# Optimization experiments

Hardware: AMD Instinct MI355X
Metric: run time of the kernel (lower is better)

The kernel has to match this reference:

```python
import jax, jax.numpy as jnp
import numpy as np

B, C_IN, C_OUT, STYLE_DIM, H, W = 8, 512, 512, 512, 32, 32

def setup_inputs() -> dict:
    key = jax.random.key(0)
    k = jax.random.split(key, 7)
    x = jax.random.normal(k[0], (B, C_IN, H, W), dtype=jnp.float32)
    style = jax.random.normal(k[1], (B, STYLE_DIM), dtype=jnp.float32)
    noise = jax.random.normal(k[2], (B, 1, 2 * H, 2 * W), dtype=jnp.float32)
    # learned params (Conv2d weight, style_fc Linear, output bias)
    conv_w = jax.random.normal(k[3], (C_OUT, C_IN, 3, 3), dtype=jnp.float32) * 0.05
    fc_w = jax.random.normal(k[4], (C_IN, STYLE_DIM), dtype=jnp.float32) * 0.05
    fc_b = jax.random.normal(k[5], (C_IN,), dtype=jnp.float32) * 0.05
    bias = jnp.zeros((1, C_OUT, 1, 1), dtype=jnp.float32)
    return {"x": x, "style": style, "noise": noise,
            "conv_w": conv_w, "fc_w": fc_w, "fc_b": fc_b, "bias": bias}

def reference(x, style, noise, conv_w, fc_w, fc_b, bias):
    b, c, h, w = x.shape
    o = conv_w.shape[0]
    x = jnp.repeat(jnp.repeat(x, 2, axis=2), 2, axis=3)  # (B, C, 2H, 2W)
    # style modulation: (B, C)
    s = style @ fc_w.T + fc_b
    # per-sample modulated weight (B, O, C, 3, 3)
    wmod = conv_w[None] * (s[:, None, :, None, None] + 1.0)
    # demodulation
    d = jax.lax.rsqrt(jnp.sum(wmod * wmod, axis=(2, 3, 4)) + 1e-8)  # (B, O)
    wmod = wmod * d[:, :, None, None, None]
    # grouped conv: one group per batch sample
    xr = x.reshape(1, b * c, 2 * h, 2 * w)
    wr = wmod.reshape(b * o, c, 3, 3)
    y = jax.lax.conv_general_dilated(
        xr, wr, window_strides=(1, 1), padding='SAME',
        feature_group_count=b,
        dimension_numbers=('NCHW', 'OIHW', 'NCHW'))
    y = y.reshape(b, o, 2 * h, 2 * w) + bias + noise
    return jax.nn.leaky_relu(y, negative_slope=0.2)
```

## Files before the change

### kernel.cpp

```cpp
#include <hip/hip_runtime.h>

typedef short v8s __attribute__((ext_vector_type(8)));
typedef float f32x4 __attribute__((ext_vector_type(4)));
typedef unsigned short ushort_t;

#define BB    8
#define CIN   512
#define COUT  512
#define SDIM  512

#define GLDS(g, l)                                                      \
    __builtin_amdgcn_global_load_lds(                                   \
        (const __attribute__((address_space(1))) void*)(g),             \
        (__attribute__((address_space(3))) void*)(l), 16, 0, 0)

static __device__ __forceinline__ ushort_t f2bf(float f) {
    union { float f; unsigned u; } un; un.f = f;
    unsigned r = un.u + 0x7FFF + ((un.u >> 16) & 1);
    return (ushort_t)(r >> 16);
}

__global__ void k_prep1(const float* __restrict__ style, const float* __restrict__ fc_w,
                        const float* __restrict__ fc_b, float* __restrict__ m,
                        const float* __restrict__ conv_w, float* __restrict__ q,
                        ushort_t* __restrict__ Wb, float* __restrict__ guard) {
    __shared__ float sst[SDIM];
    const int bid = blockIdx.x;
    if (bid < 1024) {
        const int idx = bid * 256 + threadIdx.x;
        const int o = idx >> 9, c = idx & 511;
        float w[3][3];
        const float* wp = conv_w + idx * 9;
        float qs = 0.f;
        for (int i = 0; i < 3; i++)
            for (int j = 0; j < 3; j++) {
                float v = wp[i * 3 + j];
                w[i][j] = v;
                qs += v * v;
            }
        q[idx] = qs;
        const int ch = c >> 5, kg = (c >> 3) & 3, c8 = c & 7;
        for (int py = 0; py < 2; py++) {
            float rs[2][3];
            for (int kx = 0; kx < 3; kx++) {
                rs[0][kx] = (py == 0) ? w[0][kx] : w[0][kx] + w[1][kx];
                rs[1][kx] = (py == 0) ? w[1][kx] + w[2][kx] : w[2][kx];
            }
            for (int px = 0; px < 2; px++) {
                const int p = py * 2 + px;
                float vals[4];
                if (px == 0) {
                    vals[0] = rs[0][0];
                    vals[1] = rs[0][1] + rs[0][2];
                    vals[2] = rs[1][0];
                    vals[3] = rs[1][1] + rs[1][2];
                } else {
                    vals[0] = rs[0][0] + rs[0][1];
                    vals[1] = rs[0][2];
                    vals[2] = rs[1][0] + rs[1][1];
                    vals[3] = rs[1][2];
                }
                for (int t = 0; t < 4; t++)
                    Wb[(size_t)p * (16 * 4 * 4 * 512 * 8) + (size_t)ch * (4 * 4 * 512 * 8)
                       + ((size_t)(t * 4 + kg) * 512 + o) * 8 + c8] = f2bf(vals[t]);
            }
        }
    } else {
        const int sb = bid - 1024;
        const int bx = sb & 1, b = sb >> 1;
        if (sb == 0 && threadIdx.x < 8) guard[threadIdx.x] = 0.f;
        for (int k = threadIdx.x; k < SDIM; k += 256) sst[k] = style[b * SDIM + k];
        __syncthreads();
        const int c = bx * 256 + threadIdx.x;
        float acc = fc_b[c];
        const float* wr = fc_w + c * SDIM;
        for (int k = 0; k < SDIM; k += 4) {
            float4 w4 = *(const float4*)(wr + k);
            acc += w4.x * sst[k] + w4.y * sst[k + 1] + w4.z * sst[k + 2] + w4.w * sst[k + 3];
        }
        m[b * CIN + c] = acc + 1.0f;
    }
}

__global__ void k_prep2(const float* __restrict__ x, const float* __restrict__ m,
                        ushort_t* __restrict__ Xt, const float* __restrict__ q,
                        float* __restrict__ d) {
    __shared__ __align__(16) ushort_t lt[32 * 528];
    const int bid = blockIdx.x, t = threadIdx.x;
    if (bid < 256) {
        const int r = bid & 31, b = bid >> 5;
        for (int s = t; s < 4096; s += 256) {
            const int c = s >> 3, q4 = (s & 7) * 4;
            float4 v = *(const float4*)(x + (((size_t)(b * CIN + c) * 32 + r) * 32 + q4));
            const float mv = m[b * CIN + c];
            lt[(q4 + 0) * 528 + c] = f2bf(v.x * mv);
            lt[(q4 + 1) * 528 + c] = f2bf(v.y * mv);
            lt[(q4 + 2) * 528 + c] = f2bf(v.z * mv);
            lt[(q4 + 3) * 528 + c] = f2bf(v.w * mv);
        }
        __syncthreads();
        for (int s = t; s < 2048; s += 256) {
            const int qq = s >> 6, c8 = s & 63;
            v8s v = *(v8s*)&lt[qq * 528 + c8 * 8];
            *(v8s*)(Xt + (((size_t)(b * 32 + r) * 32 + qq) * 512 + c8 * 8)) = v;
        }
    } else {
        const int w = (bid - 256) * 4 + (t >> 6);
        const int L = t & 63;
        const int b = w >> 9, o = w & 511;
        float4 q1 = *(const float4*)(q + o * 512 + L * 8);
        float4 q2 = *(const float4*)(q + o * 512 + L * 8 + 4);
        float4 m1 = *(const float4*)(m + b * 512 + L * 8);
        float4 m2 = *(const float4*)(m + b * 512 + L * 8 + 4);
        float acc = m1.x * m1.x * q1.x + m1.y * m1.y * q1.y + m1.z * m1.z * q1.z +
                    m1.w * m1.w * q1.w + m2.x * m2.x * q2.x + m2.y * m2.y * q2.y +
                    m2.z * m2.z * q2.z + m2.w * m2.w * q2.w;
        for (int off = 32; off; off >>= 1) acc += __shfl_down(acc, off, 64);
        if (L == 0) d[w] = rsqrtf(acc + 1e-8f);
    }
}

__global__ __launch_bounds__(256, 2) void k_gemm(
    const ushort_t* __restrict__ Xt, const ushort_t* __restrict__ Wb,
    const float* __restrict__ dmod, const float* __restrict__ bias,
    const float* __restrict__ noise, float* __restrict__ out,
    const float* __restrict__ guard) {
    __shared__ __align__(16) ushort_t Wt[2][128 * 64];
    __shared__ __align__(16) ushort_t Xs[2][128 * 64];

    const int tid = threadIdx.x;
    const int L = tid & 63;
    const int wid = tid >> 6;

    const int lin = blockIdx.x + 4 * blockIdx.y + 32 * blockIdx.z;
    const int log = (lin & 7) * 128 + (lin >> 3);
    const int o0 = (log & 3) * 128;
    const int r0 = ((log >> 2) & 7) * 4;
    const int zz = log >> 5;
    const int b = zz >> 2, p = zz & 3;

    const int py = p >> 1, px = p & 1;
    const int ry0 = py ? 0 : -1, cx0 = px ? 0 : -1;
    const int wo = (wid >> 1) * 64, wn = (wid & 1) * 64;
    const int l15 = L & 15, l4 = L >> 4;

    const ushort_t* XtB = Xt + (size_t)b * (32 * 32 * 512);
    const ushort_t* WbP = Wb + (size_t)p * (16 * 4 * 4 * 512 * 8);

    f32x4 acc[4][4];
#pragma unroll
    for (int i = 0; i < 4; i++)
#pragma unroll
        for (int j = 0; j < 4; j++) acc[i][j] = {0.f, 0.f, 0.f, 0.f};

    auto stage = [&](int c0, ushort_t* wbuf, ushort_t* xbuf) {
#pragma unroll
        for (int i = 0; i < 4; i++) {
            const int slot0 = i * 256 + (tid & 192);
            const int slot = i * 256 + tid;
            const int row = slot >> 3;
            const int k16 = (slot & 7) ^ (row & 7);
            const int tp = k16 >> 1;
            const int cg = c0 + (k16 & 1) * 8;
            const ushort_t* wsrc =
                WbP + (size_t)(cg >> 5) * (4 * 4 * 512 * 8)
                + ((size_t)((tp * 4 + ((cg >> 3) & 3)) * 512 + o0 + row)) * 8;
            GLDS(wsrc, wbuf + (size_t)slot0 * 8);
            const int gr = r0 + (row >> 5) + ry0 + (tp >> 1);
            const int gq = (row & 31) + cx0 + (tp & 1);
            const ushort_t* xsrc =
                ((unsigned)gr < 32u && (unsigned)gq < 32u)
                    ? XtB + (size_t)((gr * 32 + gq) * 512 + cg)
                    : (const ushort_t*)guard;
            GLDS(xsrc, xbuf + (size_t)slot0 * 8);
        }
    };

    stage(0, Wt[0], Xs[0]);
    __syncthreads();

    const int swz = (l15 & 7) << 3;
    int cur = 0;
    for (int c0 = 0; c0 < CIN; c0 += 16) {
        if (c0 + 16 < CIN) stage(c0 + 16, Wt[cur ^ 1], Xs[cur ^ 1]);
        const ushort_t* wbuf = Wt[cur];
        const ushort_t* xbuf = Xs[cur];
#pragma unroll
        for (int s = 0; s < 2; s++) {
            const int ko = (s * 32 + l4 * 8) ^ swz;
            v8s af[4], bfr[4];
#pragma unroll
            for (int i = 0; i < 4; i++)
                af[i] = *(const v8s*)&wbuf[(wo + i * 16 + l15) * 64 + ko];
#pragma unroll
            for (int j = 0; j < 4; j++)
                bfr[j] = *(const v8s*)&xbuf[(wn + j * 16 + l15) * 64 + ko];
#pragma unroll
            for (int i = 0; i < 4; i++)
#pragma unroll
                for (int j = 0; j < 4; j++)
                    acc[i][j] = __builtin_amdgcn_mfma_f32_16x16x32_bf16(
                        af[i], bfr[j], acc[i][j], 0, 0, 0);
        }
        __syncthreads();
        cur ^= 1;
    }

    const float* db = dmod + b * COUT;
    float nz[4];
    int ooff[4];
#pragma unroll
    for (int j = 0; j < 4; j++) {
        const int n = wn + j * 16 + l15;
        const int Y = 2 * (r0 + (n >> 5)) + py, X = 2 * (n & 31) + px;
        nz[j] = noise[b * 4096 + Y * 64 + X];
        ooff[j] = Y * 64 + X;
    }
    float* outB = out + (size_t)b * COUT * 4096;
#pragma unroll
    for (int i = 0; i < 4; i++) {
        const int ob = o0 + wo + i * 16 + l4 * 4;
        float4 d4 = *(const float4*)(db + ob);
        float4 b4 = *(const float4*)(bias + ob);
        const float dv[4] = {d4.x, d4.y, d4.z, d4.w};
        const float bv[4] = {b4.x, b4.y, b4.z, b4.w};
#pragma unroll
        for (int reg = 0; reg < 4; reg++) {
            float* orow = outB + (size_t)(ob + reg) * 4096;
#pragma unroll
            for (int j = 0; j < 4; j++) {
                float v = acc[i][j][reg] * dv[reg] + bv[reg] + nz[j];
                orow[ooff[j]] = v > 0.f ? v : 0.2f * v;
            }
        }
    }
}

extern "C" void kernel_launch(void* const* d_in, const int* in_sizes, int n_in,
                              void* d_out, int out_size, void* d_ws, size_t ws_size,
                              hipStream_t stream) {
    const float* x      = (const float*)d_in[0];
    const float* style  = (const float*)d_in[1];
    const float* noise  = (const float*)d_in[2];
    const float* conv_w = (const float*)d_in[3];
    const float* fc_w   = (const float*)d_in[4];
    const float* fc_b   = (const float*)d_in[5];
    const float* bias   = (const float*)d_in[6];
    float* out = (float*)d_out;

    float* ws = (float*)d_ws;
    float* m     = ws;
    float* dmod  = ws + 4096;
    float* q     = ws + 8192;
    float* guard = ws + 270336;
    ushort_t* XtU = (ushort_t*)(ws + 270352);
    ushort_t* WbU = XtU + 4194304;

    k_prep1<<<1040, 256, 0, stream>>>(style, fc_w, fc_b, m, conv_w, q, WbU, guard);
    k_prep2<<<1280, 256, 0, stream>>>(x, m, XtU, q, dmod);
    k_gemm<<<dim3(4, 8, 32), 256, 0, stream>>>(XtU, WbU, dmod, bias, noise, out, guard);
}
```

Measured before the change: 226.6 us.

## Enlarge GEMM tiles to 256x256 with 32x32 MFMA and interleaved staging

```diff
diff --git a/kernel.cpp b/kernel.cpp
--- a/kernel.cpp
+++ b/kernel.cpp
@@ -2,6 +2,7 @@
 
 typedef short v8s __attribute__((ext_vector_type(8)));
 typedef float f32x4 __attribute__((ext_vector_type(4)));
+typedef float f32x16 __attribute__((ext_vector_type(16)));
 typedef unsigned short ushort_t;
 
 #define BB    8
@@ -120,117 +121,146 @@
     }
 }
 
-__global__ __launch_bounds__(256, 2) void k_gemm(
+__global__ __launch_bounds__(512, 2) void k_gemm(
     const ushort_t* __restrict__ Xt, const ushort_t* __restrict__ Wb,
     const float* __restrict__ dmod, const float* __restrict__ bias,
     const float* __restrict__ noise, float* __restrict__ out,
     const float* __restrict__ guard) {
-    __shared__ __align__(16) ushort_t Wt[2][128 * 64];
-    __shared__ __align__(16) ushort_t Xs[2][128 * 64];
+    __shared__ __align__(16) ushort_t Wt[2][256 * 64];
+    __shared__ __align__(16) ushort_t Xs[2][256 * 64];
 
     const int tid = threadIdx.x;
     const int L = tid & 63;
     const int wid = tid >> 6;
 
-    const int lin = blockIdx.x + 4 * blockIdx.y + 32 * blockIdx.z;
-    const int log = (lin & 7) * 128 + (lin >> 3);
-    const int o0 = (log & 3) * 128;
-    const int r0 = ((log >> 2) & 7) * 4;
-    const int zz = log >> 5;
+    const int lin = blockIdx.x + 2 * blockIdx.y + 8 * blockIdx.z;
+    const int log = (lin & 7) * 32 + (lin >> 3);
+    const int o0 = (log & 1) * 256;
+    const int n0 = ((log >> 1) & 3) * 256;
+    const int zz = log >> 3;
     const int b = zz >> 2, p = zz & 3;
 
     const int py = p >> 1, px = p & 1;
     const int ry0 = py ? 0 : -1, cx0 = px ? 0 : -1;
-    const int wo = (wid >> 1) * 64, wn = (wid & 1) * 64;
-    const int l15 = L & 15, l4 = L >> 4;
+    const int wo = (wid >> 2) * 128, wn = (wid & 3) * 64;
+    const int l31 = L & 31, h = L >> 5;
 
     const ushort_t* XtB = Xt + (size_t)b * (32 * 32 * 512);
     const ushort_t* WbP = Wb + (size_t)p * (16 * 4 * 4 * 512 * 8);
 
-    f32x4 acc[4][4];
+    f32x16 acc[4][2];
 #pragma unroll
     for (int i = 0; i < 4; i++)
 #pragma unroll
-        for (int j = 0; j < 4; j++) acc[i][j] = {0.f, 0.f, 0.f, 0.f};
-
-    auto stage = [&](int c0, ushort_t* wbuf, ushort_t* xbuf) {
+        for (int j = 0; j < 2; j++)
+#pragma unroll
+            for (int r = 0; r < 16; r++) acc[i][j][r] = 0.f;
+
+    auto stage_w = [&](int c0, ushort_t* wbuf) {
 #pragma unroll
         for (int i = 0; i < 4; i++) {
-            const int slot0 = i * 256 + (tid & 192);
-            const int slot = i * 256 + tid;
+            const int slot = i * 512 + tid;
             const int row = slot >> 3;
-            const int k16 = (slot & 7) ^ (row & 7);
-            const int tp = k16 >> 1;
-            const int cg = c0 + (k16 & 1) * 8;
+            const int g = (slot & 7) ^ (row & 7);
+            const int tap = g >> 1;
+            const int cg = c0 + (g & 1) * 8;
             const ushort_t* wsrc =
                 WbP + (size_t)(cg >> 5) * (4 * 4 * 512 * 8)
-                + ((size_t)((tp * 4 + ((cg >> 3) & 3)) * 512 + o0 + row)) * 8;
-            GLDS(wsrc, wbuf + (size_t)slot0 * 8);
-            const int gr = r0 + (row >> 5) + ry0 + (tp >> 1);
-            const int gq = (row & 31) + cx0 + (tp & 1);
+                + ((size_t)((tap * 4 + ((cg >> 3) & 3)) * 512 + o0 + row)) * 8;
+            GLDS(wsrc, wbuf + (size_t)(i * 512 + (tid & 448)) * 8);
+        }
+    };
+    auto stage_x = [&](int c0, ushort_t* xbuf) {
+#pragma unroll
+        for (int i = 0; i < 4; i++) {
+            const int slot = i * 512 + tid;
+            const int row = slot >> 3;
+            const int g = (slot & 7) ^ (row & 7);
+            const int tap = g >> 1;
+            const int cg = c0 + (g & 1) * 8;
+            const int pix = n0 + row;
+            const int gr = (pix >> 5) + ry0 + (tap >> 1);
+            const int gq = (pix & 31) + cx0 + (tap & 1);
             const ushort_t* xsrc =
                 ((unsigned)gr < 32u && (unsigned)gq < 32u)
                     ? XtB + (size_t)((gr * 32 + gq) * 512 + cg)
                     : (const ushort_t*)guard;
-            GLDS(xsrc, xbuf + (size_t)slot0 * 8);
+            GLDS(xsrc, xbuf + (size_t)(i * 512 + (tid & 448)) * 8);
         }
     };
 
-    stage(0, Wt[0], Xs[0]);
+    stage_w(0, Wt[0]);
+    stage_x(0, Xs[0]);
+    asm volatile("s_waitcnt vmcnt(0)" ::: "memory");
     __syncthreads();
 
-    const int swz = (l15 & 7) << 3;
     int cur = 0;
-    for (int c0 = 0; c0 < CIN; c0 += 16) {
-        if (c0 + 16 < CIN) stage(c0 + 16, Wt[cur ^ 1], Xs[cur ^ 1]);
-        const ushort_t* wbuf = Wt[cur];
-        const ushort_t* xbuf = Xs[cur];
-#pragma unroll
-        for (int s = 0; s < 2; s++) {
-            const int ko = (s * 32 + l4 * 8) ^ swz;
-            v8s af[4], bfr[4];
+    for (int t = 0; t < 32; ++t) {
+        const ushort_t* wb = Wt[cur];
+        const ushort_t* xb = Xs[cur];
+        const int c0n = (t + 1) * 16;
+#pragma unroll
+        for (int s = 0; s < 4; ++s) {
+            v8s af[4], bfr[2];
+            const int ga = (2 * s + h) ^ (l31 & 7);
+#pragma unroll
+            for (int i = 0; i < 4; i++) {
+                const int row = wo + i * 32 + l31;
+                af[i] = *(const v8s*)&wb[row * 64 + ga * 8];
+            }
+#pragma unroll
+            for (int j = 0; j < 2; j++) {
+                const int row = wn + j * 32 + l31;
+                bfr[j] = *(const v8s*)&xb[row * 64 + ga * 8];
+            }
+            if (t < 31) {
+                if (s == 0) stage_w(c0n, Wt[cur ^ 1]);
+                else if (s == 1) stage_x(c0n, Xs[cur ^ 1]);
+            }
+            __builtin_amdgcn_s_barrier();
+            __builtin_amdgcn_s_setprio(1);
 #pragma unroll
             for (int i = 0; i < 4; i++)
-                af[i] = *(const v8s*)&wbuf[(wo + i * 16 + l15) * 64 + ko];
-#pragma unroll
-            for (int j = 0; j < 4; j++)
-                bfr[j] = *(const v8s*)&xbuf[(wn + j * 16 + l15) * 64 + ko];
-#pragma unroll
-            for (int i = 0; i < 4; i++)
-#pragma unroll
-                for (int j = 0; j < 4; j++)
-                    acc[i][j] = __builtin_amdgcn_mfma_f32_16x16x32_bf16(
+#pragma unroll
+                for (int j = 0; j < 2; j++)
+                    acc[i][j] = __builtin_amdgcn_mfma_f32_32x32x16_bf16(
                         af[i], bfr[j], acc[i][j], 0, 0, 0);
-        }
-        __syncthreads();
+            __builtin_amdgcn_s_setprio(0);
+            if (s == 3) asm volatile("s_waitcnt vmcnt(0)" ::: "memory");
+            __builtin_amdgcn_s_barrier();
+        }
         cur ^= 1;
     }
 
     const float* db = dmod + b * COUT;
-    float nz[4];
-    int ooff[4];
-#pragma unroll
-    for (int j = 0; j < 4; j++) {
-        const int n = wn + j * 16 + l15;
-        const int Y = 2 * (r0 + (n >> 5)) + py, X = 2 * (n & 31) + px;
+    float nz[2];
+    int ooff[2];
+#pragma unroll
+    for (int j = 0; j < 2; j++) {
+        const int pix = n0 + wn + j * 32 + l31;
+        const int Y = 2 * (pix >> 5) + py, X = 2 * (pix & 31) + px;
         nz[j] = noise[b * 4096 + Y * 64 + X];
         ooff[j] = Y * 64 + X;
     }
     float* outB = out + (size_t)b * COUT * 4096;
 #pragma unroll
     for (int i = 0; i < 4; i++) {
-        const int ob = o0 + wo + i * 16 + l4 * 4;
-        float4 d4 = *(const float4*)(db + ob);
-        float4 b4 = *(const float4*)(bias + ob);
-        const float dv[4] = {d4.x, d4.y, d4.z, d4.w};
-        const float bv[4] = {b4.x, b4.y, b4.z, b4.w};
-#pragma unroll
-        for (int reg = 0; reg < 4; reg++) {
-            float* orow = outB + (size_t)(ob + reg) * 4096;
-#pragma unroll
-            for (int j = 0; j < 4; j++) {
-                float v = acc[i][j][reg] * dv[reg] + bv[reg] + nz[j];
-                orow[ooff[j]] = v > 0.f ? v : 0.2f * v;
+#pragma unroll
+        for (int rq = 0; rq < 4; rq++) {
+            const int ob = o0 + wo + i * 32 + rq * 8 + h * 4;
+            float4 d4 = *(const float4*)(db + ob);
+            float4 b4 = *(const float4*)(bias + ob);
+            const float dv[4] = {d4.x, d4.y, d4.z, d4.w};
+            const float bv[4] = {b4.x, b4.y, b4.z, b4.w};
+#pragma unroll
+            for (int rr = 0; rr < 4; rr++) {
+                const int reg = rq * 4 + rr;
+                float* orow = outB + (size_t)(ob + rr) * 4096;
+#pragma unroll
+                for (int j = 0; j < 2; j++) {
+                    float v = acc[i][j][reg] * dv[rr] + bv[rr] + nz[j];
+                    orow[ooff[j]] = v > 0.f ? v : 0.2f * v;
+                }
             }
         }
     }
@@ -258,5 +288,5 @@
 
     k_prep1<<<1040, 256, 0, stream>>>(style, fc_w, fc_b, m, conv_w, q, WbU, guard);
     k_prep2<<<1280, 256, 0, stream>>>(x, m, XtU, q, dmod);
-    k_gemm<<<dim3(4, 8, 32), 256, 0, stream>>>(XtU, WbU, dmod, bias, noise, out, guard);
-}
+    k_gemm<<<dim3(2, 4, 32), 512, 0, stream>>>(XtU, WbU, dmod, bias, noise, out, guard);
+}
```

Result: faster. 216.3 us (-4.5%).

## Enlarge GEMM tile to 256x256 with 4-stage LDS pipeline and MFMA priority

Applied to the files above, without the earlier changes.

```diff
diff --git a/kernel.cpp b/kernel.cpp
--- a/kernel.cpp
+++ b/kernel.cpp
@@ -120,90 +120,121 @@
     }
 }
 
-__global__ __launch_bounds__(256, 2) void k_gemm(
+__global__ __launch_bounds__(512, 2) void k_gemm(
     const ushort_t* __restrict__ Xt, const ushort_t* __restrict__ Wb,
     const float* __restrict__ dmod, const float* __restrict__ bias,
     const float* __restrict__ noise, float* __restrict__ out,
     const float* __restrict__ guard) {
-    __shared__ __align__(16) ushort_t Wt[2][128 * 64];
-    __shared__ __align__(16) ushort_t Xs[2][128 * 64];
+    __shared__ __align__(16) ushort_t Wt[4][256 * 32];
+    __shared__ __align__(16) ushort_t Xs[4][256 * 32];
 
     const int tid = threadIdx.x;
     const int L = tid & 63;
     const int wid = tid >> 6;
 
-    const int lin = blockIdx.x + 4 * blockIdx.y + 32 * blockIdx.z;
-    const int log = (lin & 7) * 128 + (lin >> 3);
-    const int o0 = (log & 3) * 128;
-    const int r0 = ((log >> 2) & 7) * 4;
-    const int zz = log >> 5;
+    const int lin = blockIdx.x + 2 * blockIdx.y + 8 * blockIdx.z;
+    const int log = (lin & 7) * 32 + (lin >> 3);
+    const int o0 = (log & 1) * 256;
+    const int n0 = ((log >> 1) & 3) * 256;
+    const int zz = log >> 3;
     const int b = zz >> 2, p = zz & 3;
 
     const int py = p >> 1, px = p & 1;
     const int ry0 = py ? 0 : -1, cx0 = px ? 0 : -1;
-    const int wo = (wid >> 1) * 64, wn = (wid & 1) * 64;
+    const int wo = (wid >> 2) * 128, wn = (wid & 3) * 64;
     const int l15 = L & 15, l4 = L >> 4;
 
     const ushort_t* XtB = Xt + (size_t)b * (32 * 32 * 512);
     const ushort_t* WbP = Wb + (size_t)p * (16 * 4 * 4 * 512 * 8);
 
-    f32x4 acc[4][4];
-#pragma unroll
-    for (int i = 0; i < 4; i++)
+    f32x4 acc[8][4];
+#pragma unroll
+    for (int i = 0; i < 8; i++)
 #pragma unroll
         for (int j = 0; j < 4; j++) acc[i][j] = {0.f, 0.f, 0.f, 0.f};
 
-    auto stage = [&](int c0, ushort_t* wbuf, ushort_t* xbuf) {
-#pragma unroll
-        for (int i = 0; i < 4; i++) {
-            const int slot0 = i * 256 + (tid & 192);
-            const int slot = i * 256 + tid;
-            const int row = slot >> 3;
-            const int k16 = (slot & 7) ^ (row & 7);
-            const int tp = k16 >> 1;
-            const int cg = c0 + (k16 & 1) * 8;
-            const ushort_t* wsrc =
-                WbP + (size_t)(cg >> 5) * (4 * 4 * 512 * 8)
-                + ((size_t)((tp * 4 + ((cg >> 3) & 3)) * 512 + o0 + row)) * 8;
-            GLDS(wsrc, wbuf + (size_t)slot0 * 8);
-            const int gr = r0 + (row >> 5) + ry0 + (tp >> 1);
-            const int gq = (row & 31) + cx0 + (tp & 1);
-            const ushort_t* xsrc =
-                ((unsigned)gr < 32u && (unsigned)gq < 32u)
-                    ? XtB + (size_t)((gr * 32 + gq) * 512 + cg)
-                    : (const ushort_t*)guard;
-            GLDS(xsrc, xbuf + (size_t)slot0 * 8);
-        }
+    auto stage1 = [&](int c0, ushort_t* wbuf, ushort_t* xbuf, int i) {
+        const int slot = i * 512 + tid;
+        const int row = slot >> 2;
+        const int tap = (slot & 3) ^ ((row >> 1) & 3);
+        const int ldo = (i * 512 + (tid & 448)) * 8;
+        const ushort_t* wsrc =
+            WbP + (size_t)(c0 >> 5) * (4 * 4 * 512 * 8)
+            + ((size_t)((tap * 4 + ((c0 >> 3) & 3)) * 512 + o0 + row)) * 8;
+        GLDS(wsrc, wbuf + ldo);
+        const int pix = n0 + row;
+        const int gr = (pix >> 5) + ry0 + (tap >> 1);
+        const int gq = (pix & 31) + cx0 + (tap & 1);
+        const ushort_t* xsrc =
+            ((unsigned)gr < 32u && (unsigned)gq < 32u)
+                ? XtB + (size_t)((gr * 32 + gq) * 512 + c0)
+                : (const ushort_t*)guard;
+        GLDS(xsrc, xbuf + ldo);
     };
 
-    stage(0, Wt[0], Xs[0]);
-    __syncthreads();
-
-    const int swz = (l15 & 7) << 3;
-    int cur = 0;
-    for (int c0 = 0; c0 < CIN; c0 += 16) {
-        if (c0 + 16 < CIN) stage(c0 + 16, Wt[cur ^ 1], Xs[cur ^ 1]);
-        const ushort_t* wbuf = Wt[cur];
-        const ushort_t* xbuf = Xs[cur];
-#pragma unroll
-        for (int s = 0; s < 2; s++) {
-            const int ko = (s * 32 + l4 * 8) ^ swz;
-            v8s af[4], bfr[4];
-#pragma unroll
-            for (int i = 0; i < 4; i++)
-                af[i] = *(const v8s*)&wbuf[(wo + i * 16 + l15) * 64 + ko];
-#pragma unroll
-            for (int j = 0; j < 4; j++)
-                bfr[j] = *(const v8s*)&xbuf[(wn + j * 16 + l15) * 64 + ko];
+    auto lread = [&](const ushort_t* buf, int row) -> v8s {
+        const int gsel = l4 ^ ((row >> 1) & 3);
+        return *(const v8s*)&buf[row * 32 + gsel * 8];
+    };
+
+#pragma unroll
+    for (int pt = 0; pt < 3; ++pt) {
+        stage1(pt * 8, Wt[pt], Xs[pt], 0);
+        stage1(pt * 8, Wt[pt], Xs[pt], 1);
+    }
+    asm volatile("s_waitcnt vmcnt(8)" ::: "memory");
+    __builtin_amdgcn_s_barrier();
+
+    v8s bfr[4];
+    for (int t = 0; t < 64; ++t) {
+        const ushort_t* wb = Wt[t & 3];
+        const ushort_t* xb = Xs[t & 3];
+        ushort_t* wnb = Wt[(t + 3) & 3];
+        ushort_t* xnb = Xs[(t + 3) & 3];
+        const int c0n = (t + 3) * 8;
+        const bool st = (t + 3) < 64;
+
+        {
+            v8s af[4];
+#pragma unroll
+            for (int i = 0; i < 4; i++) af[i] = lread(wb, wo + i * 16 + l15);
+#pragma unroll
+            for (int j = 0; j < 4; j++) bfr[j] = lread(xb, wn + j * 16 + l15);
+            if (st) stage1(c0n, wnb, xnb, 0);
+            __builtin_amdgcn_s_barrier();
+            asm volatile("s_waitcnt lgkmcnt(0)" ::: "memory");
+            __builtin_amdgcn_sched_barrier(0);
+            __builtin_amdgcn_s_setprio(1);
 #pragma unroll
             for (int i = 0; i < 4; i++)
 #pragma unroll
                 for (int j = 0; j < 4; j++)
                     acc[i][j] = __builtin_amdgcn_mfma_f32_16x16x32_bf16(
                         af[i], bfr[j], acc[i][j], 0, 0, 0);
-        }
-        __syncthreads();
-        cur ^= 1;
+            __builtin_amdgcn_s_setprio(0);
+            __builtin_amdgcn_s_barrier();
+        }
+        {
+            v8s af[4];
+#pragma unroll
+            for (int i = 0; i < 4; i++) af[i] = lread(wb, wo + 64 + i * 16 + l15);
+            if (st) stage1(c0n, wnb, xnb, 1);
+            __builtin_amdgcn_s_barrier();
+            asm volatile("s_waitcnt lgkmcnt(0)" ::: "memory");
+            __builtin_amdgcn_sched_barrier(0);
+            __builtin_amdgcn_s_setprio(1);
+#pragma unroll
+            for (int i = 0; i < 4; i++)
+#pragma unroll
+                for (int j = 0; j < 4; j++)
+                    acc[4 + i][j] = __builtin_amdgcn_mfma_f32_16x16x32_bf16(
+                        af[i], bfr[j], acc[4 + i][j], 0, 0, 0);
+            __builtin_amdgcn_s_setprio(0);
+            if (t <= 60) asm volatile("s_waitcnt vmcnt(8)" ::: "memory");
+            else if (t == 61) asm volatile("s_waitcnt vmcnt(4)" ::: "memory");
+            else if (t == 62) asm volatile("s_waitcnt vmcnt(0)" ::: "memory");
+            __builtin_amdgcn_s_barrier();
+        }
     }
 
     const float* db = dmod + b * COUT;
@@ -211,14 +242,14 @@
     int ooff[4];
 #pragma unroll
     for (int j = 0; j < 4; j++) {
-        const int n = wn + j * 16 + l15;
-        const int Y = 2 * (r0 + (n >> 5)) + py, X = 2 * (n & 31) + px;
+        const int pix = n0 + wn + j * 16 + l15;
+        const int Y = 2 * (pix >> 5) + py, X = 2 * (pix & 31) + px;
         nz[j] = noise[b * 4096 + Y * 64 + X];
         ooff[j] = Y * 64 + X;
     }
     float* outB = out + (size_t)b * COUT * 4096;
 #pragma unroll
-    for (int i = 0; i < 4; i++) {
+    for (int i = 0; i < 8; i++) {
         const int ob = o0 + wo + i * 16 + l4 * 4;
         float4 d4 = *(const float4*)(db + ob);
         float4 b4 = *(const float4*)(bias + ob);
@@ -258,5 +289,5 @@
 
     k_prep1<<<1040, 256, 0, stream>>>(style, fc_w, fc_b, m, conv_w, q, WbU, guard);
     k_prep2<<<1280, 256, 0, stream>>>(x, m, XtU, q, dmod);
-    k_gemm<<<dim3(4, 8, 32), 256, 0, stream>>>(XtU, WbU, dmod, bias, noise, out, guard);
-}
+    k_gemm<<<dim3(2, 4, 32), 512, 0, stream>>>(XtU, WbU, dmod, bias, noise, out, guard);
+}
```

Result: faster. 202.0 us (-10.9%).
